# Kernel optimization log

Measured on AMD Instinct MI355X. Metric: run time of the kernel, lower is better.

The kernel has to match this reference:

```python
import jax, jax.numpy as jnp
import numpy as np

APERTURE = 256
IGNORE_ITSELF = False
FMAX = jnp.float32(3.4028235e38)  # tf.float32.max


def setup_inputs() -> dict:
    key = jax.random.key(0)
    ks = jax.random.split(key, 5)
    n, m, d = 4096, 1024, 1024
    scale = 1.0 / np.sqrt(m)
    x = jax.random.normal(ks[0], (n, m), dtype=jnp.float32)
    WK = jax.random.normal(ks[1], (m, d), dtype=jnp.float32) * scale
    WQ = jax.random.normal(ks[2], (m, d), dtype=jnp.float32) * scale
    WV = jax.random.normal(ks[3], (m, d), dtype=jnp.float32) * scale
    Wout = jax.random.normal(ks[4], (d, m), dtype=jnp.float32) * scale
    return {"x": x, "WK": WK, "WQ": WQ, "WV": WV, "Wout": Wout}


def reference(x, WK, WQ, WV, Wout):
    n = x.shape[0]
    K = x @ WK                      # [n, d]
    Q = (x @ WQ) * 0.06             # [n, d]
    V = x @ WV                      # [n, d]
    logits = Q @ K.T                # [n, n]

    i = jnp.arange(n)[:, None]
    j = jnp.arange(n)[None, :]
    if IGNORE_ITSELF:
        keep = (i != j).astype(jnp.float32)
        logits = logits * keep - FMAX * (1.0 - keep)
    if APERTURE > 0:
        # tf: mask = 1 - band_part(ones, -aperture, aperture); negative num_lower
        # keeps the whole lower triangle, so mask==1 exactly where j - i > aperture.
        keep = (j - i > APERTURE).astype(jnp.float32)
        logits = logits * keep - FMAX * (1.0 - keep)

    att_weights = jax.nn.softmax(logits, axis=-1)  # [n, n]
    # dropout is identity (training=False). NOTE faithful quirk: transpose_a=True.
    y = att_weights.T @ V           # [n, d]
    y = y @ Wout                    # [n, m]
    return (y, att_weights)
```

## Files before the change

### kernel.cpp

```cpp
#include <hip/hip_runtime.h>
#include <cstdint>
#include <cstddef>

#define N_TOK 4096
#define M_DIM 1024
#define APER  256
#define UNIF_START 3839

typedef __attribute__((ext_vector_type(8))) short short8;
typedef __attribute__((ext_vector_type(4))) float float4_t;

__device__ __forceinline__ unsigned short f2bf(float x) {
    union { float f; uint32_t u; } v; v.f = x;
    uint32_t u = v.u;
    u += 0x7FFFu + ((u >> 16) & 1u);
    return (unsigned short)(u >> 16);
}

__device__ __forceinline__ void gload16(const void* g, void* l) {
    __builtin_amdgcn_global_load_lds(
        (const __attribute__((address_space(1))) void*)g,
        (__attribute__((address_space(3))) void*)l, 16, 0, 0);
}

__global__ __launch_bounds__(256) void cast_bf16(const float* __restrict__ src,
                                                 unsigned short* __restrict__ dst, int n) {
    const int i = (blockIdx.x * 256 + threadIdx.x) * 4;
    if (i >= n) return;
    const float4 v = *reinterpret_cast<const float4*>(&src[i]);
    ushort4 o;
    o.x = f2bf(v.x); o.y = f2bf(v.y); o.z = f2bf(v.z); o.w = f2bf(v.w);
    *reinterpret_cast<ushort4*>(&dst[i]) = o;
}

__global__ __launch_bounds__(256) void wtrans3(const float* __restrict__ W0, const float* __restrict__ W1,
                                               const float* __restrict__ W2,
                                               unsigned short* __restrict__ D0, unsigned short* __restrict__ D1,
                                               unsigned short* __restrict__ D2) {
    const int z = blockIdx.z;
    const float* src = z == 0 ? W0 : (z == 1 ? W1 : W2);
    unsigned short* dst = z == 0 ? D0 : (z == 1 ? D1 : D2);
    __shared__ unsigned short tile[32][33];
    const int c0 = blockIdx.x * 32, r0 = blockIdx.y * 32;
    const int tx = threadIdx.x & 31, ty = threadIdx.x >> 5;
#pragma unroll
    for (int i = ty; i < 32; i += 8)
        tile[i][tx] = f2bf(src[(size_t)(r0 + i) * M_DIM + c0 + tx]);
    __syncthreads();
#pragma unroll
    for (int i = ty; i < 32; i += 8)
        dst[(size_t)(c0 + i) * M_DIM + r0 + tx] = tile[tx][i];
}

__global__ __launch_bounds__(256) void transpose_bf16(const unsigned short* __restrict__ src,
                                                      unsigned short* __restrict__ dst,
                                                      int R, int C) {
    __shared__ unsigned short tile[32][33];
    const int c0 = blockIdx.x * 32, r0 = blockIdx.y * 32;
    const int tx = threadIdx.x & 31, ty = threadIdx.x >> 5;
#pragma unroll
    for (int i = ty; i < 32; i += 8)
        tile[i][tx] = src[(size_t)(r0 + i) * C + c0 + tx];
    __syncthreads();
#pragma unroll
    for (int i = ty; i < 32; i += 8)
        dst[(size_t)(c0 + i) * R + r0 + tx] = tile[tx][i];
}

template <int SKIP>
__global__ __launch_bounds__(256) void nt64sq(const unsigned short* __restrict__ A,
                                              const unsigned short* __restrict__ B,
                                              float* __restrict__ Cf,
                                              unsigned short* __restrict__ Cb,
                                              int N, int K) {
    const int by   = (SKIP == 1) ? ((int)gridDim.y - 1 - (int)blockIdx.y) : (int)blockIdx.y;
    const int row0 = by * 64;
    const int col0 = blockIdx.x * 64;

    __shared__ unsigned short Asb[64 * 32];
    __shared__ unsigned short Bsb[64 * 32];

    const int t = threadIdx.x, w = t >> 6, lane = t & 63;
    float4_t acc[4] = {};

    const int sr   = lane >> 2;
    const int sk   = ((lane & 3) ^ ((sr >> 1) & 3)) * 8;
    const int m    = lane & 15;
    const int slot = ((lane >> 4) ^ ((m >> 1) & 3)) * 8;

    for (int k0 = 0; k0 < K; k0 += 32) {
        if (SKIP == 1) {
            if ((k0 > row0 + 63 - APER - 1) && (k0 + 31 < UNIF_START)) continue;
        }
        const int rr = w * 16 + sr;
        gload16(&A[(size_t)(row0 + rr) * K + k0 + sk], &Asb[w * 512]);
        gload16(&B[(size_t)(col0 + rr) * K + k0 + sk], &Bsb[w * 512]);
        __syncthreads();
        const short8 af = *reinterpret_cast<const short8*>(&Asb[(w * 16 + m) * 32 + slot]);
        short8 bf[4];
#pragma unroll
        for (int j = 0; j < 4; ++j)
            bf[j] = *reinterpret_cast<const short8*>(&Bsb[(j * 16 + m) * 32 + slot]);
#pragma unroll
        for (int j = 0; j < 4; ++j)
            acc[j] = __builtin_amdgcn_mfma_f32_16x16x32_bf16(af, bf[j], acc[j], 0, 0, 0);
        __syncthreads();
    }

    const int crow = row0 + w * 16 + (lane >> 4) * 4;
    const int ccol = col0 + m;
#pragma unroll
    for (int j = 0; j < 4; ++j)
#pragma unroll
        for (int r = 0; r < 4; ++r) {
            const float v = acc[j][r];
            const size_t idx = (size_t)(crow + r) * N + ccol + j * 16;
            if (Cf) Cf[idx] = v;
            if (Cb) Cb[idx] = f2bf(v);
        }
}

__global__ __launch_bounds__(256) void mfma_qkv(const unsigned short* __restrict__ xb,
                                                const unsigned short* __restrict__ WKt,
                                                const unsigned short* __restrict__ WQt,
                                                const unsigned short* __restrict__ WVWt,
                                                unsigned short* __restrict__ Kb,
                                                unsigned short* __restrict__ Qb,
                                                unsigned short* __restrict__ VWb) {
    const int row0  = blockIdx.y * 128;
    const int col0g = blockIdx.x * 128;
    const int seg   = col0g >> 10;
    const int col0  = col0g & 1023;
    const unsigned short* B = seg == 0 ? WKt : (seg == 1 ? WQt : WVWt);
    unsigned short*       C = seg == 0 ? Kb  : (seg == 1 ? Qb  : VWb);
    const float alpha = (seg == 1) ? 0.06f : 1.0f;

    __shared__ unsigned short Asb[128 * 32];
    __shared__ unsigned short Bsb[128 * 32];

    const int t = threadIdx.x, w = t >> 6, lane = t & 63;
    const int wr = (w >> 1) * 64, wc = (w & 1) * 64;

    float4_t acc[4][4] = {};

    const int sr   = lane >> 2;
    const int sk   = ((lane & 3) ^ ((sr >> 1) & 3)) * 8;
    const int m    = lane & 15;
    const int slot = ((lane >> 4) ^ ((m >> 1) & 3)) * 8;

    for (int k0 = 0; k0 < M_DIM; k0 += 32) {
#pragma unroll
        for (int cc = 0; cc < 2; ++cc) {
            const int c = 2 * w + cc;
            const int rr = c * 16 + sr;
            gload16(&xb[(size_t)(row0 + rr) * M_DIM + k0 + sk], &Asb[c * 512]);
            gload16(&B[(size_t)(col0 + rr) * M_DIM + k0 + sk], &Bsb[c * 512]);
        }
        __syncthreads();
        short8 af[4], bf[4];
#pragma unroll
        for (int i = 0; i < 4; ++i)
            af[i] = *reinterpret_cast<const short8*>(&Asb[(wr + i * 16 + m) * 32 + slot]);
#pragma unroll
        for (int j = 0; j < 4; ++j)
            bf[j] = *reinterpret_cast<const short8*>(&Bsb[(wc + j * 16 + m) * 32 + slot]);
#pragma unroll
        for (int i = 0; i < 4; ++i)
#pragma unroll
            for (int j = 0; j < 4; ++j)
                acc[i][j] = __builtin_amdgcn_mfma_f32_16x16x32_bf16(af[i], bf[j], acc[i][j], 0, 0, 0);
        __syncthreads();
    }

    const int crow = row0 + wr + (lane >> 4) * 4;
    const int ccol = col0 + wc + m;
#pragma unroll
    for (int i = 0; i < 4; ++i)
#pragma unroll
        for (int j = 0; j < 4; ++j)
#pragma unroll
            for (int r = 0; r < 4; ++r)
                C[(size_t)(crow + i * 16 + r) * M_DIM + ccol + j * 16] = f2bf(alpha * acc[i][j][r]);
}

__global__ __launch_bounds__(256) void mfma_logits_exp(const unsigned short* __restrict__ A,
                                                       const unsigned short* __restrict__ B,
                                                       float* __restrict__ att,
                                                       float* __restrict__ rowsum) {
    const int row0 = blockIdx.y * 128;
    const int col0 = blockIdx.x * 128;
    if (col0 + 127 <= row0 + APER) return;

    __shared__ unsigned short Asb[128 * 32];
    __shared__ unsigned short Bsb[128 * 32];

    const int t = threadIdx.x, w = t >> 6, lane = t & 63;
    const int wr = (w >> 1) * 64, wc = (w & 1) * 64;

    float4_t acc[4][4] = {};

    const int sr   = lane >> 2;
    const int sk   = ((lane & 3) ^ ((sr >> 1) & 3)) * 8;
    const int m    = lane & 15;
    const int slot = ((lane >> 4) ^ ((m >> 1) & 3)) * 8;

    for (int k0 = 0; k0 < M_DIM; k0 += 32) {
#pragma unroll
        for (int cc = 0; cc < 2; ++cc) {
            const int c = 2 * w + cc;
            const int rr = c * 16 + sr;
            gload16(&A[(size_t)(row0 + rr) * M_DIM + k0 + sk], &Asb[c * 512]);
            gload16(&B[(size_t)(col0 + rr) * M_DIM + k0 + sk], &Bsb[c * 512]);
        }
        __syncthreads();
        short8 af[4], bf[4];
#pragma unroll
        for (int i = 0; i < 4; ++i)
            af[i] = *reinterpret_cast<const short8*>(&Asb[(wr + i * 16 + m) * 32 + slot]);
#pragma unroll
        for (int j = 0; j < 4; ++j)
            bf[j] = *reinterpret_cast<const short8*>(&Bsb[(wc + j * 16 + m) * 32 + slot]);
#pragma unroll
        for (int i = 0; i < 4; ++i)
#pragma unroll
            for (int j = 0; j < 4; ++j)
                acc[i][j] = __builtin_amdgcn_mfma_f32_16x16x32_bf16(af[i], bf[j], acc[i][j], 0, 0, 0);
        __syncthreads();
    }

    const int crow = row0 + wr + (lane >> 4) * 4;
    const int ccol = col0 + wc + m;
#pragma unroll
    for (int i = 0; i < 4; ++i) {
#pragma unroll
        for (int r = 0; r < 4; ++r) {
            const int gr = crow + i * 16 + r;
            float partial = 0.0f;
#pragma unroll
            for (int j = 0; j < 4; ++j) {
                const int gc = ccol + j * 16;
                float val;
                if (gr >= UNIF_START) {
                    val = 1.0f;
                } else if (gc > gr + APER) {
                    val = __expf(acc[i][j][r]);
                    partial += val;
                } else {
                    val = 0.0f;
                }
                att[(size_t)gr * N_TOK + gc] = val;
            }
            partial += __shfl_xor(partial, 1, 64);
            partial += __shfl_xor(partial, 2, 64);
            partial += __shfl_xor(partial, 4, 64);
            partial += __shfl_xor(partial, 8, 64);
            if (m == 0 && gr < UNIF_START) atomicAdd(&rowsum[gr], partial);
        }
    }
}

__global__ __launch_bounds__(256) void init_rowsum(float* __restrict__ rowsum) {
    const int i = blockIdx.x * 256 + threadIdx.x;
    if (i < N_TOK) rowsum[i] = (i >= UNIF_START) ? (float)N_TOK : 0.0f;
}

__global__ __launch_bounds__(256) void finalize_att(float* __restrict__ att,
                                                    unsigned short* __restrict__ attT,
                                                    const float* __restrict__ rowsum) {
    const int j0 = blockIdx.x * 64, i0 = blockIdx.y * 64;
    const int t = threadIdx.x;
    const int rl = t >> 4;
    const int c4 = (t & 15) * 4;
    const float u = 1.0f / (float)N_TOK;

    if (j0 + 63 <= i0 + APER) {
#pragma unroll
        for (int s = 0; s < 4; ++s) {
            const int i = i0 + rl + 16 * s;
            const float val = (i >= UNIF_START) ? u : 0.0f;
            float4 v; v.x = v.y = v.z = v.w = val;
            *reinterpret_cast<float4*>(&att[(size_t)i * N_TOK + j0 + c4]) = v;
        }
        const unsigned short bu = f2bf(u);
#pragma unroll
        for (int s = 0; s < 4; ++s) {
            const int j = j0 + rl + 16 * s;
            ushort4 o;
            o.x = (i0 + c4 + 0 >= UNIF_START) ? bu : 0;
            o.y = (i0 + c4 + 1 >= UNIF_START) ? bu : 0;
            o.z = (i0 + c4 + 2 >= UNIF_START) ? bu : 0;
            o.w = (i0 + c4 + 3 >= UNIF_START) ? bu : 0;
            *reinterpret_cast<ushort4*>(&attT[(size_t)j * N_TOK + i0 + c4]) = o;
        }
        return;
    }

    __shared__ unsigned short tile[64][72];
#pragma unroll
    for (int s = 0; s < 4; ++s) {
        const int il = rl + 16 * s;
        const int i  = i0 + il;
        const float inv = 1.0f / rowsum[i];
        float4 v = *reinterpret_cast<const float4*>(&att[(size_t)i * N_TOK + j0 + c4]);
        v.x *= inv; v.y *= inv; v.z *= inv; v.w *= inv;
        *reinterpret_cast<float4*>(&att[(size_t)i * N_TOK + j0 + c4]) = v;
        ushort4 b;
        b.x = f2bf(v.x); b.y = f2bf(v.y); b.z = f2bf(v.z); b.w = f2bf(v.w);
        *reinterpret_cast<ushort4*>(&tile[il][c4]) = b;
    }
    __syncthreads();
#pragma unroll
    for (int s = 0; s < 4; ++s) {
        const int jl = rl + 16 * s;
        ushort4 o;
        o.x = tile[c4 + 0][jl];
        o.y = tile[c4 + 1][jl];
        o.z = tile[c4 + 2][jl];
        o.w = tile[c4 + 3][jl];
        *reinterpret_cast<ushort4*>(&attT[(size_t)(j0 + jl) * N_TOK + i0 + c4]) = o;
    }
}

extern "C" void kernel_launch(void* const* d_in, const int* in_sizes, int n_in,
                              void* d_out, int out_size, void* d_ws, size_t ws_size,
                              hipStream_t stream) {
    const float* x    = (const float*)d_in[0];
    const float* WK   = (const float*)d_in[1];
    const float* WQ   = (const float*)d_in[2];
    const float* WV   = (const float*)d_in[3];
    const float* Wout = (const float*)d_in[4];

    float* y   = (float*)d_out;
    float* att = y + (size_t)N_TOK * M_DIM;

    unsigned short* base = (unsigned short*)d_ws;
    const size_t MEG = 1u << 20;
    unsigned short* xb    = base;
    unsigned short* WKt   = base + 4  * MEG;
    unsigned short* WQt   = base + 5  * MEG;
    unsigned short* Woutt = base + 6  * MEG;
    unsigned short* WVb   = base + 7  * MEG;
    unsigned short* WVWt  = base + 8  * MEG;
    unsigned short* Kb    = base + 9  * MEG;
    unsigned short* Qb    = base + 13 * MEG;
    unsigned short* VWb   = base + 17 * MEG;
    unsigned short* attT  = base + 4  * MEG;
    float*          rowsum = (float*)(base + 20 * MEG);
    unsigned short* VWt   = xb;

    const dim3 blk(256);

    cast_bf16<<<dim3((N_TOK * M_DIM) / 1024), blk, 0, stream>>>(x, xb, N_TOK * M_DIM);
    cast_bf16<<<dim3((M_DIM * M_DIM) / 1024), blk, 0, stream>>>(WV, WVb, M_DIM * M_DIM);
    wtrans3<<<dim3(M_DIM / 32, M_DIM / 32, 3), blk, 0, stream>>>(WK, WQ, Wout, WKt, WQt, Woutt);

    nt64sq<0><<<dim3(M_DIM / 64, M_DIM / 64), blk, 0, stream>>>(Woutt, WVb, nullptr, WVWt,
                                                                M_DIM, M_DIM);

    mfma_qkv<<<dim3(24, N_TOK / 128), blk, 0, stream>>>(xb, WKt, WQt, WVWt, Kb, Qb, VWb);

    transpose_bf16<<<dim3(M_DIM / 32, N_TOK / 32), blk, 0, stream>>>(VWb, VWt, N_TOK, M_DIM);

    init_rowsum<<<dim3(N_TOK / 256), blk, 0, stream>>>(rowsum);
    mfma_logits_exp<<<dim3(N_TOK / 128, N_TOK / 128), blk, 0, stream>>>(Qb, Kb, att, rowsum);

    finalize_att<<<dim3(N_TOK / 64, N_TOK / 64), blk, 0, stream>>>(att, attT, rowsum);

    nt64sq<1><<<dim3(M_DIM / 64, N_TOK / 64), blk, 0, stream>>>(attT, VWt, y, nullptr,
                                                                M_DIM, N_TOK);
}
```

Baseline: 290.1 us.

## Fuse prep kernels, transpose VW in QKV epilogue, halve logits tile rows

Merges the cast, weight-transpose and rowsum-init kernels into one prep launch. The QKV GEMM now writes the V·W segment already transposed through an LDS staging tile, which removes the separate transpose kernel. The logits kernel uses 64-row tiles so more blocks run and the triangular skip is finer-grained. Together these cut launch count and a full read/write pass over VW. The cost is more per-block overhead in the logits GEMM, since each B tile is reused across fewer rows.

```diff
diff --git a/kernel.cpp b/kernel.cpp
--- a/kernel.cpp
+++ b/kernel.cpp
@@ -23,48 +23,55 @@
         (__attribute__((address_space(3))) void*)l, 16, 0, 0);
 }
 
-__global__ __launch_bounds__(256) void cast_bf16(const float* __restrict__ src,
-                                                 unsigned short* __restrict__ dst, int n) {
-    const int i = (blockIdx.x * 256 + threadIdx.x) * 4;
-    if (i >= n) return;
-    const float4 v = *reinterpret_cast<const float4*>(&src[i]);
-    ushort4 o;
-    o.x = f2bf(v.x); o.y = f2bf(v.y); o.z = f2bf(v.z); o.w = f2bf(v.w);
-    *reinterpret_cast<ushort4*>(&dst[i]) = o;
-}
-
-__global__ __launch_bounds__(256) void wtrans3(const float* __restrict__ W0, const float* __restrict__ W1,
-                                               const float* __restrict__ W2,
-                                               unsigned short* __restrict__ D0, unsigned short* __restrict__ D1,
-                                               unsigned short* __restrict__ D2) {
-    const int z = blockIdx.z;
-    const float* src = z == 0 ? W0 : (z == 1 ? W1 : W2);
-    unsigned short* dst = z == 0 ? D0 : (z == 1 ? D1 : D2);
+__global__ __launch_bounds__(256) void prep(const float* __restrict__ x,
+                                            const float* __restrict__ WK,
+                                            const float* __restrict__ WQ,
+                                            const float* __restrict__ WV,
+                                            const float* __restrict__ Wout,
+                                            unsigned short* __restrict__ xb,
+                                            unsigned short* __restrict__ WKt,
+                                            unsigned short* __restrict__ WQt,
+                                            unsigned short* __restrict__ WVb,
+                                            unsigned short* __restrict__ Woutt,
+                                            float* __restrict__ rowsum) {
+    const int bx = blockIdx.x;
+    const int t  = threadIdx.x;
     __shared__ unsigned short tile[32][33];
-    const int c0 = blockIdx.x * 32, r0 = blockIdx.y * 32;
-    const int tx = threadIdx.x & 31, ty = threadIdx.x >> 5;
-#pragma unroll
-    for (int i = ty; i < 32; i += 8)
-        tile[i][tx] = f2bf(src[(size_t)(r0 + i) * M_DIM + c0 + tx]);
-    __syncthreads();
-#pragma unroll
-    for (int i = ty; i < 32; i += 8)
-        dst[(size_t)(c0 + i) * M_DIM + r0 + tx] = tile[tx][i];
-}
-
-__global__ __launch_bounds__(256) void transpose_bf16(const unsigned short* __restrict__ src,
-                                                      unsigned short* __restrict__ dst,
-                                                      int R, int C) {
-    __shared__ unsigned short tile[32][33];
-    const int c0 = blockIdx.x * 32, r0 = blockIdx.y * 32;
-    const int tx = threadIdx.x & 31, ty = threadIdx.x >> 5;
-#pragma unroll
-    for (int i = ty; i < 32; i += 8)
-        tile[i][tx] = src[(size_t)(r0 + i) * C + c0 + tx];
-    __syncthreads();
-#pragma unroll
-    for (int i = ty; i < 32; i += 8)
-        dst[(size_t)(c0 + i) * R + r0 + tx] = tile[tx][i];
+
+    if (bx < 4096) {
+        const int i = (bx * 256 + t) * 4;
+        const float4 v = *reinterpret_cast<const float4*>(&x[i]);
+        ushort4 o;
+        o.x = f2bf(v.x); o.y = f2bf(v.y); o.z = f2bf(v.z); o.w = f2bf(v.w);
+        *reinterpret_cast<ushort4*>(&xb[i]) = o;
+        return;
+    }
+    if (bx < 7168) {
+        const int z = (bx - 4096) >> 10;
+        const int l = (bx - 4096) & 1023;
+        const float* src = z == 0 ? WK : (z == 1 ? WQ : Wout);
+        unsigned short* dst = z == 0 ? WKt : (z == 1 ? WQt : Woutt);
+        const int c0 = (l & 31) * 32, r0 = (l >> 5) * 32;
+        const int tx = t & 31, ty = t >> 5;
+#pragma unroll
+        for (int i = ty; i < 32; i += 8)
+            tile[i][tx] = f2bf(src[(size_t)(r0 + i) * M_DIM + c0 + tx]);
+        __syncthreads();
+#pragma unroll
+        for (int i = ty; i < 32; i += 8)
+            dst[(size_t)(c0 + i) * M_DIM + r0 + tx] = tile[tx][i];
+        return;
+    }
+    if (bx < 8192) {
+        const int i = ((bx - 7168) * 256 + t) * 4;
+        const float4 v = *reinterpret_cast<const float4*>(&WV[i]);
+        ushort4 o;
+        o.x = f2bf(v.x); o.y = f2bf(v.y); o.z = f2bf(v.z); o.w = f2bf(v.w);
+        *reinterpret_cast<ushort4*>(&WVb[i]) = o;
+        return;
+    }
+    const int i = (bx - 8192) * 256 + t;
+    if (i < N_TOK) rowsum[i] = (i >= UNIF_START) ? (float)N_TOK : 0.0f;
 }
 
 template <int SKIP>
@@ -126,17 +133,18 @@
                                                 const unsigned short* __restrict__ WVWt,
                                                 unsigned short* __restrict__ Kb,
                                                 unsigned short* __restrict__ Qb,
-                                                unsigned short* __restrict__ VWb) {
+                                                unsigned short* __restrict__ VWt) {
     const int row0  = blockIdx.y * 128;
     const int col0g = blockIdx.x * 128;
     const int seg   = col0g >> 10;
     const int col0  = col0g & 1023;
     const unsigned short* B = seg == 0 ? WKt : (seg == 1 ? WQt : WVWt);
-    unsigned short*       C = seg == 0 ? Kb  : (seg == 1 ? Qb  : VWb);
     const float alpha = (seg == 1) ? 0.06f : 1.0f;
 
-    __shared__ unsigned short Asb[128 * 32];
-    __shared__ unsigned short Bsb[128 * 32];
+    __shared__ union {
+        struct { unsigned short A[128 * 32]; unsigned short B[128 * 32]; } s;
+        unsigned short T[64][136];
+    } sm;
 
     const int t = threadIdx.x, w = t >> 6, lane = t & 63;
     const int wr = (w >> 1) * 64, wc = (w & 1) * 64;
@@ -146,24 +154,25 @@
     const int sr   = lane >> 2;
     const int sk   = ((lane & 3) ^ ((sr >> 1) & 3)) * 8;
     const int m    = lane & 15;
-    const int slot = ((lane >> 4) ^ ((m >> 1) & 3)) * 8;
+    const int q    = lane >> 4;
+    const int slot = (q ^ ((m >> 1) & 3)) * 8;
 
     for (int k0 = 0; k0 < M_DIM; k0 += 32) {
 #pragma unroll
         for (int cc = 0; cc < 2; ++cc) {
             const int c = 2 * w + cc;
             const int rr = c * 16 + sr;
-            gload16(&xb[(size_t)(row0 + rr) * M_DIM + k0 + sk], &Asb[c * 512]);
-            gload16(&B[(size_t)(col0 + rr) * M_DIM + k0 + sk], &Bsb[c * 512]);
+            gload16(&xb[(size_t)(row0 + rr) * M_DIM + k0 + sk], &sm.s.A[c * 512]);
+            gload16(&B[(size_t)(col0 + rr) * M_DIM + k0 + sk], &sm.s.B[c * 512]);
         }
         __syncthreads();
         short8 af[4], bf[4];
 #pragma unroll
         for (int i = 0; i < 4; ++i)
-            af[i] = *reinterpret_cast<const short8*>(&Asb[(wr + i * 16 + m) * 32 + slot]);
+            af[i] = *reinterpret_cast<const short8*>(&sm.s.A[(wr + i * 16 + m) * 32 + slot]);
 #pragma unroll
         for (int j = 0; j < 4; ++j)
-            bf[j] = *reinterpret_cast<const short8*>(&Bsb[(wc + j * 16 + m) * 32 + slot]);
+            bf[j] = *reinterpret_cast<const short8*>(&sm.s.B[(wc + j * 16 + m) * 32 + slot]);
 #pragma unroll
         for (int i = 0; i < 4; ++i)
 #pragma unroll
@@ -172,66 +181,96 @@
         __syncthreads();
     }
 
-    const int crow = row0 + wr + (lane >> 4) * 4;
-    const int ccol = col0 + wc + m;
-#pragma unroll
-    for (int i = 0; i < 4; ++i)
-#pragma unroll
-        for (int j = 0; j < 4; ++j)
-#pragma unroll
-            for (int r = 0; r < 4; ++r)
-                C[(size_t)(crow + i * 16 + r) * M_DIM + ccol + j * 16] = f2bf(alpha * acc[i][j][r]);
+    if (seg < 2) {
+        unsigned short* C = seg == 0 ? Kb : Qb;
+        const int crow = row0 + wr + q * 4;
+        const int ccol = col0 + wc + m;
+#pragma unroll
+        for (int i = 0; i < 4; ++i)
+#pragma unroll
+            for (int j = 0; j < 4; ++j)
+#pragma unroll
+                for (int r = 0; r < 4; ++r)
+                    C[(size_t)(crow + i * 16 + r) * M_DIM + ccol + j * 16] = f2bf(alpha * acc[i][j][r]);
+        return;
+    }
+
+#pragma unroll
+    for (int h = 0; h < 2; ++h) {
+        __syncthreads();
+        if ((w & 1) == h) {
+#pragma unroll
+            for (int i = 0; i < 4; ++i)
+#pragma unroll
+                for (int j = 0; j < 4; ++j)
+#pragma unroll
+                    for (int r = 0; r < 4; ++r)
+                        sm.T[m + j * 16][wr + q * 4 + i * 16 + r] = f2bf(acc[i][j][r]);
+        }
+        __syncthreads();
+#pragma unroll
+        for (int rr = 0; rr < 8; ++rr) {
+            const int cl = w * 16 + rr * 2 + (lane >> 5);
+            const int il = (lane & 31) * 4;
+            *reinterpret_cast<ushort4*>(&VWt[(size_t)(col0 + h * 64 + cl) * N_TOK + row0 + il]) =
+                *reinterpret_cast<const ushort4*>(&sm.T[cl][il]);
+        }
+    }
 }
 
 __global__ __launch_bounds__(256) void mfma_logits_exp(const unsigned short* __restrict__ A,
                                                        const unsigned short* __restrict__ B,
                                                        float* __restrict__ att,
                                                        float* __restrict__ rowsum) {
-    const int row0 = blockIdx.y * 128;
+    const int row0 = blockIdx.y * 64;
     const int col0 = blockIdx.x * 128;
     if (col0 + 127 <= row0 + APER) return;
 
-    __shared__ unsigned short Asb[128 * 32];
+    __shared__ unsigned short Asb[64 * 32];
     __shared__ unsigned short Bsb[128 * 32];
 
     const int t = threadIdx.x, w = t >> 6, lane = t & 63;
-    const int wr = (w >> 1) * 64, wc = (w & 1) * 64;
-
-    float4_t acc[4][4] = {};
+    const int wr = (w >> 1) * 32, wc = (w & 1) * 64;
+
+    float4_t acc[2][4] = {};
 
     const int sr   = lane >> 2;
     const int sk   = ((lane & 3) ^ ((sr >> 1) & 3)) * 8;
     const int m    = lane & 15;
-    const int slot = ((lane >> 4) ^ ((m >> 1) & 3)) * 8;
+    const int q    = lane >> 4;
+    const int slot = (q ^ ((m >> 1) & 3)) * 8;
 
     for (int k0 = 0; k0 < M_DIM; k0 += 32) {
+        {
+            const int rr = w * 16 + sr;
+            gload16(&A[(size_t)(row0 + rr) * M_DIM + k0 + sk], &Asb[w * 512]);
+        }
 #pragma unroll
         for (int cc = 0; cc < 2; ++cc) {
             const int c = 2 * w + cc;
             const int rr = c * 16 + sr;
-            gload16(&A[(size_t)(row0 + rr) * M_DIM + k0 + sk], &Asb[c * 512]);
             gload16(&B[(size_t)(col0 + rr) * M_DIM + k0 + sk], &Bsb[c * 512]);
         }
         __syncthreads();
-        short8 af[4], bf[4];
-#pragma unroll
-        for (int i = 0; i < 4; ++i)
+        short8 af[2], bf[4];
+#pragma unroll
+        for (int i = 0; i < 2; ++i)
             af[i] = *reinterpret_cast<const short8*>(&Asb[(wr + i * 16 + m) * 32 + slot]);
 #pragma unroll
         for (int j = 0; j < 4; ++j)
             bf[j] = *reinterpret_cast<const short8*>(&Bsb[(wc + j * 16 + m) * 32 + slot]);
 #pragma unroll
-        for (int i = 0; i < 4; ++i)
+        for (int i = 0; i < 2; ++i)
 #pragma unroll
             for (int j = 0; j < 4; ++j)
                 acc[i][j] = __builtin_amdgcn_mfma_f32_16x16x32_bf16(af[i], bf[j], acc[i][j], 0, 0, 0);
         __syncthreads();
     }
 
-    const int crow = row0 + wr + (lane >> 4) * 4;
+    const int crow = row0 + wr + q * 4;
     const int ccol = col0 + wc + m;
 #pragma unroll
-    for (int i = 0; i < 4; ++i) {
+    for (int i = 0; i < 2; ++i) {
 #pragma unroll
         for (int r = 0; r < 4; ++r) {
             const int gr = crow + i * 16 + r;
@@ -259,11 +298,6 @@
     }
 }
 
-__global__ __launch_bounds__(256) void init_rowsum(float* __restrict__ rowsum) {
-    const int i = blockIdx.x * 256 + threadIdx.x;
-    if (i < N_TOK) rowsum[i] = (i >= UNIF_START) ? (float)N_TOK : 0.0f;
-}
-
 __global__ __launch_bounds__(256) void finalize_att(float* __restrict__ att,
                                                     unsigned short* __restrict__ attT,
                                                     const float* __restrict__ rowsum) {
@@ -343,26 +377,20 @@
     unsigned short* WVWt  = base + 8  * MEG;
     unsigned short* Kb    = base + 9  * MEG;
     unsigned short* Qb    = base + 13 * MEG;
-    unsigned short* VWb   = base + 17 * MEG;
-    unsigned short* attT  = base + 4  * MEG;
-    float*          rowsum = (float*)(base + 20 * MEG);
-    unsigned short* VWt   = xb;
+    unsigned short* VWt   = base + 17 * MEG;
+    unsigned short* attT  = base;
+    float*          rowsum = (float*)(base + 21 * MEG);
 
     const dim3 blk(256);
 
-    cast_bf16<<<dim3((N_TOK * M_DIM) / 1024), blk, 0, stream>>>(x, xb, N_TOK * M_DIM);
-    cast_bf16<<<dim3((M_DIM * M_DIM) / 1024), blk, 0, stream>>>(WV, WVb, M_DIM * M_DIM);
-    wtrans3<<<dim3(M_DIM / 32, M_DIM / 32, 3), blk, 0, stream>>>(WK, WQ, Wout, WKt, WQt, Woutt);
+    prep<<<dim3(8208), blk, 0, stream>>>(x, WK, WQ, WV, Wout, xb, WKt, WQt, WVb, Woutt, rowsum);
 
     nt64sq<0><<<dim3(M_DIM / 64, M_DIM / 64), blk, 0, stream>>>(Woutt, WVb, nullptr, WVWt,
                                                                 M_DIM, M_DIM);
 
-    mfma_qkv<<<dim3(24, N_TOK / 128), blk, 0, stream>>>(xb, WKt, WQt, WVWt, Kb, Qb, VWb);
-
-    transpose_bf16<<<dim3(M_DIM / 32, N_TOK / 32), blk, 0, stream>>>(VWb, VWt, N_TOK, M_DIM);
-
-    init_rowsum<<<dim3(N_TOK / 256), blk, 0, stream>>>(rowsum);
-    mfma_logits_exp<<<dim3(N_TOK / 128, N_TOK / 128), blk, 0, stream>>>(Qb, Kb, att, rowsum);
+    mfma_qkv<<<dim3(24, N_TOK / 128), blk, 0, stream>>>(xb, WKt, WQt, WVWt, Kb, Qb, VWt);
+
+    mfma_logits_exp<<<dim3(N_TOK / 128, N_TOK / 64), blk, 0, stream>>>(Qb, Kb, att, rowsum);
 
     finalize_att<<<dim3(N_TOK / 64, N_TOK / 64), blk, 0, stream>>>(att, attT, rowsum);
 
```

New measurement: 299.3 us. 3.1% more time.
